# Kernel optimization log

Hardware: AMD Instinct MI355X
Metric: run time of the kernel (lower is better)

Reference implementation:

```python
import jax, jax.numpy as jnp
import numpy as np

NUM_CLASSES = 80
NUM_ANCHORS = 5
INPUT_SIZE = 6656
GRID = 208
CONF_THR = 0.5
IOU_THR = 0.5
TOPK = 1024  # pre-NMS cap (fixed-shape stand-in for the dynamic python NMS loop)
ANCHORS = np.array([[1.3221, 1.73145], [3.19275, 4.00944], [5.05587, 8.09892],
                    [9.47112, 4.84053], [11.2364, 10.0071]], dtype=np.float32)


def setup_inputs() -> dict:
    key = jax.random.key(0)
    x = jax.random.normal(key, (1, NUM_ANCHORS * (5 + NUM_CLASSES), GRID, GRID), dtype=jnp.float32)
    return {"x": x, "scaled_anchors": jnp.asarray(ANCHORS)}


def _decode(x, anchors):
    B, C, H, W = x.shape
    A = anchors.shape[0]
    stride_h = INPUT_SIZE / H
    stride_w = INPUT_SIZE / W
    # [B, A, H, W, 5+nc]
    p = x.reshape(B, A, C // A, H, W).transpose(0, 1, 3, 4, 2)
    bx = jax.nn.sigmoid(p[..., 0]) + jnp.arange(W, dtype=x.dtype)[None, None, None, :]
    by = jax.nn.sigmoid(p[..., 1]) + jnp.arange(H, dtype=x.dtype)[None, None, :, None]
    bw = jnp.exp(p[..., 2]) * anchors[:, 0][None, :, None, None]
    bh = jnp.exp(p[..., 3]) * anchors[:, 1][None, :, None, None]
    conf = jax.nn.sigmoid(p[..., 4])
    # original applies sigmoid then argmax; sigmoid is monotone so argmax of logits is identical
    cls_idx = jnp.argmax(p[..., 5:], axis=-1)
    scale = jnp.array([stride_w, stride_h, stride_w, stride_h], dtype=x.dtype)
    boxes = jnp.stack([bx, by, bw, bh], axis=-1) * scale  # [B,A,H,W,4]
    return boxes.reshape(B, -1, 4), conf.reshape(B, -1), cls_idx.reshape(B, -1)


def _iou_cxcywh(b1, b2):
    # faithful to the original intersection_over_union, including its
    # (c - s)/2 parenthesization and abs() on areas
    x1min = (b1[..., 0] - b1[..., 2]) / 2.0
    y1min = (b1[..., 1] - b1[..., 3]) / 2.0
    x1max = (b1[..., 0] + b1[..., 2]) / 2.0
    y1max = (b1[..., 1] + b1[..., 3]) / 2.0
    x2min = (b2[..., 0] - b2[..., 2]) / 2.0
    y2min = (b2[..., 1] - b2[..., 3]) / 2.0
    x2max = (b2[..., 0] + b2[..., 2]) / 2.0
    y2max = (b2[..., 1] + b2[..., 3]) / 2.0
    inter = (jnp.clip(jnp.minimum(x1max, x2max) - jnp.maximum(x1min, x2min), 0)
             * jnp.clip(jnp.minimum(y1max, y2max) - jnp.maximum(y1min, y2min), 0))
    a1 = jnp.abs((x1max - x1min) * (y1max - y1min))
    a2 = jnp.abs((x2max - x2min) * (y2max - y2min))
    return inter / (a1 + a2 - inter + 1e-6)


def _nms(boxes, conf, cls_idx):
    # conf filter + sort-by-confidence expressed as a fixed-size top_k
    scores = jnp.where(conf > CONF_THR, conf, -1.0)
    top_scores, idx = jax.lax.top_k(scores, TOPK)
    b = boxes[idx]            # [K,4]
    c = conf[idx]             # [K]
    cl = cls_idx[idx]         # [K]
    keep0 = top_scores > CONF_THR
    order = jnp.arange(TOPK)

    def body(i, keep):
        ious = _iou_cxcywh(b[i], b)                     # [K]
        suppress = (ious >= IOU_THR) & (cl == cl[i]) & (order > i)
        return jnp.where(keep[i], keep & ~suppress, keep)

    keep = jax.lax.fori_loop(0, TOPK, body, keep0)
    out = jnp.concatenate([b, c[:, None], cl[:, None].astype(b.dtype)], axis=-1)  # [K,6]
    return jnp.where(keep[:, None], out, 0.0)


def reference(x, scaled_anchors):
    boxes, conf, cls_idx = _decode(x, scaled_anchors)
    return _nms(boxes[0], conf[0], cls_idx[0])
```

## Files before the change

### kernel.cpp

```cpp
#include <hip/hip_runtime.h>
#include <stdint.h>

#define N_LOC 216320
#define PLANE 43264
#define GRIDW 208
#define NCAP 2048
#define TOPK 1024

typedef unsigned long long u64;
typedef uint32_t u32;

#define OFF_KEYS      0u
#define OFF_HIST      865280u
#define OFF_CTR       881664u
#define OFF_CAND      881696u
#define OFF_SELIDX    898080u
#define OFF_CONF      902176u
#define OFF_BOX       906272u
#define OFF_CLS       922656u
#define OFF_NZ        926752u
#define OFF_SUP       926880u

__global__ void k_init(u32* hist, u32* ctr, u64* nz, float* conf) {
    int t = blockIdx.x * 256 + threadIdx.x;
    if (t < 4096) hist[t] = 0;
    if (t < 8) ctr[t] = 0;
    if (t < 16) nz[t] = 0;
    if (t < 1024) conf[t] = 0.0f;
}

__global__ void k_scores(const float* __restrict__ x, u32* keys, u32* hist) {
    int i = blockIdx.x * 256 + threadIdx.x;
    if (i >= N_LOC) return;
    int a = i / PLANE;
    int hw = i - a * PLANE;
    float v = x[(a * 85 + 4) * PLANE + hw];
    float cf = 1.0f / (1.0f + expf(-v));
    u32 key = (cf > 0.5f) ? __float_as_uint(cf) : 0u;
    keys[i] = key;
    if (key) {
        u32 bin = (key >= 0x3F800000u) ? 4095u : ((key >> 11) & 0xFFFu);
        atomicAdd(&hist[bin], 1u);
    }
}

__global__ void k_findbin(const u32* hist, u32* ctr) {
    __shared__ u32 lhist[4096];
    __shared__ u32 csum[256];
    int t = threadIdx.x;
    u32 s = 0;
    for (int b = 0; b < 16; b++) {
        u32 h = hist[t * 16 + b];
        lhist[t * 16 + b] = h;
        s += h;
    }
    csum[t] = s;
    __syncthreads();
    if (t == 0) {
        u32 acc = 0;
        int selB = 0;
        int c = 255;
        for (; c >= 0; c--) {
            if (acc + csum[c] >= (u32)TOPK) break;
            acc += csum[c];
        }
        if (c >= 0) {
            int b = c * 16 + 15;
            for (; b >= c * 16; b--) {
                acc += lhist[b];
                if (acc >= (u32)TOPK) break;
            }
            if (b < c * 16) b = c * 16;
            selB = b;
        }
        ctr[1] = 0x3F000000u | ((u32)selB << 11);
    }
}

__global__ void k_compact(const u32* keys, u32* ctr, u64* cand) {
    int i = blockIdx.x * 256 + threadIdx.x;
    if (i >= N_LOC) return;
    u32 k = keys[i];
    u32 thr = ctr[1];
    if (k >= thr && k != 0u) {
        u32 pos = atomicAdd(&ctr[0], 1u);
        if (pos < (u32)NCAP)
            cand[pos] = ((u64)k << 32) | (u64)(~(u32)i);
    }
}

__global__ void __launch_bounds__(256) k_rank(const u32* __restrict__ ctr,
                                              const u64* __restrict__ cand,
                                              u32* sel_idx, float* conf) {
    u32 M = ctr[0];
    if (M > (u32)NCAP) M = NCAP;
    u32 b = blockIdx.x;
    if (b >= M) return;
    u64 key = cand[b];
    int t = threadIdx.x;
    u32 cnt = 0;
    for (u32 j = (u32)t; j < M; j += 256) cnt += (cand[j] > key) ? 1u : 0u;
    for (int off = 32; off; off >>= 1) cnt += __shfl_down(cnt, off);
    __shared__ u32 scnt;
    if (t == 0) scnt = 0;
    __syncthreads();
    if ((t & 63) == 0) atomicAdd(&scnt, cnt);
    __syncthreads();
    if (t == 0) {
        u32 rank = scnt;
        if (rank < (u32)TOPK) {
            sel_idx[rank] = ~((u32)key);
            conf[rank] = __uint_as_float((u32)(key >> 32));
        }
    }
}

__global__ void __launch_bounds__(256) k_decode(const float* __restrict__ x,
                                                const float* __restrict__ anchors,
                                                const u32* __restrict__ sel_idx,
                                                const float* __restrict__ conf,
                                                float4* box, float* clsf) {
    int wave = (blockIdx.x * 256 + threadIdx.x) >> 6;
    int lane = threadIdx.x & 63;
    float cf = conf[wave];
    if (cf <= 0.0f) {
        if (lane == 0) { box[wave] = make_float4(0.f, 0.f, 0.f, 0.f); clsf[wave] = 0.f; }
        return;
    }
    u32 i = sel_idx[wave];
    u32 a = i / PLANE;
    u32 hw = i - a * PLANE;
    u32 h = hw / GRIDW;
    u32 w = hw - h * GRIDW;
    const float* base = x + (size_t)(a * 85u) * PLANE + hw;
    float v0 = base[(5 + lane) * PLANE];
    int   c0 = lane;
    if (lane < 16) {
        float v1 = base[(5 + 64 + lane) * PLANE];
        if (v1 > v0) { v0 = v1; c0 = 64 + lane; }
    }
    float pv = (lane < 4) ? base[lane * PLANE] : 0.f;
    for (int off = 32; off; off >>= 1) {
        float ov = __shfl_xor(v0, off);
        int   oc = __shfl_xor(c0, off);
        if (ov > v0 || (ov == v0 && oc < c0)) { v0 = ov; c0 = oc; }
    }
    float p0 = __shfl(pv, 0);
    float p1 = __shfl(pv, 1);
    float p2 = __shfl(pv, 2);
    float p3 = __shfl(pv, 3);
    if (lane == 0) {
        float bx = (1.0f / (1.0f + expf(-p0)) + (float)w) * 32.0f;
        float by = (1.0f / (1.0f + expf(-p1)) + (float)h) * 32.0f;
        float bw = (expf(p2) * anchors[a * 2 + 0]) * 32.0f;
        float bh = (expf(p3) * anchors[a * 2 + 1]) * 32.0f;
        box[wave] = make_float4(bx, by, bw, bh);
        clsf[wave] = (float)c0;
    }
}

__global__ void __launch_bounds__(256) k_supmat(const float4* __restrict__ box,
                                                const float* __restrict__ clsf,
                                                u64* sup, u64* nz) {
    int i = blockIdx.x;
    float4 bi = box[i];
    float ci = clsf[i];
    float x1min = (bi.x - bi.z) * 0.5f, x1max = (bi.x + bi.z) * 0.5f;
    float y1min = (bi.y - bi.w) * 0.5f, y1max = (bi.y + bi.w) * 0.5f;
    float a1 = fabsf((x1max - x1min) * (y1max - y1min));
    int t = threadIdx.x;
    u64 any = 0;
    __shared__ u64 wany[4];
    for (int c = 0; c < 4; c++) {
        int j = c * 256 + t;
        bool s = false;
        if (j > i) {
            float4 bj = box[j];
            float x2min = (bj.x - bj.z) * 0.5f, x2max = (bj.x + bj.z) * 0.5f;
            float y2min = (bj.y - bj.w) * 0.5f, y2max = (bj.y + bj.w) * 0.5f;
            float iw = fmaxf(fminf(x1max, x2max) - fmaxf(x1min, x2min), 0.0f);
            float ih = fmaxf(fminf(y1max, y2max) - fmaxf(y1min, y2min), 0.0f);
            float inter = iw * ih;
            float a2 = fabsf((x2max - x2min) * (y2max - y2min));
            float iou = inter / (a1 + a2 - inter + 1e-6f);
            s = (iou >= 0.5f) && (clsf[j] == ci);
        }
        u64 msk = __ballot(s);
        if ((t & 63) == 0) sup[i * 16 + c * 4 + (t >> 6)] = msk;
        any |= msk;
    }
    if ((t & 63) == 0) wany[t >> 6] = any;
    __syncthreads();
    if (t == 0) {
        u64 tot = wany[0] | wany[1] | wany[2] | wany[3];
        if (tot) atomicOr(&nz[i >> 6], 1ull << (i & 63));
    }
}

__global__ void __launch_bounds__(1024) k_nms_out(const u64* __restrict__ sup,
                                                  const u64* __restrict__ nz,
                                                  const float4* __restrict__ box,
                                                  const float* __restrict__ conf,
                                                  const float* __restrict__ clsf,
                                                  float* __restrict__ out) {
    __shared__ u64 candLDS[16];
    __shared__ u64 remLDS[16];
    int t = threadIdx.x;
    float cf = conf[t];
    bool valid = cf > 0.0f;
    u64 bm = __ballot(valid);
    if ((t & 63) == 0) candLDS[t >> 6] = bm;
    __syncthreads();
    if (t < 64) {
        int lane = t;
        u64 rem = 0;
        u64 cnd = (lane < 16) ? candLDS[lane] : 0ull;
        u64 nzw = (lane < 16) ? nz[lane] : 0ull;
        for (int g = 0; g < 16; g++) {
            u64 myword = cnd & ~rem;
            u64 live = __shfl(myword, g);
            u64 act = live & __shfl(nzw, g);
            while (act) {
                int b = __builtin_ctzll(act);
                int i = g * 64 + b;
                u64 row = (lane < 16) ? sup[i * 16 + lane] : 0ull;
                rem |= row;
                u64 row_g = __shfl(row, g);
                act &= ~row_g;
                act &= ~(1ull << b);
            }
        }
        if (lane < 16) remLDS[lane] = rem;
    }
    __syncthreads();
    int r = t;
    u64 rw = remLDS[r >> 6];
    bool kept = valid && !((rw >> (r & 63)) & 1ull);
    float4 b4 = box[r];
    float cl = clsf[r];
    float* o = out + r * 6;
    if (kept) {
        o[0] = b4.x; o[1] = b4.y; o[2] = b4.z; o[3] = b4.w; o[4] = cf; o[5] = cl;
    } else {
        o[0] = 0.f; o[1] = 0.f; o[2] = 0.f; o[3] = 0.f; o[4] = 0.f; o[5] = 0.f;
    }
}

extern "C" void kernel_launch(void* const* d_in, const int* in_sizes, int n_in,
                              void* d_out, int out_size, void* d_ws, size_t ws_size,
                              hipStream_t stream) {
    const float* x = (const float*)d_in[0];
    const float* anchors = (const float*)d_in[1];
    float* out = (float*)d_out;
    char* ws = (char*)d_ws;

    u32* keys     = (u32*)(ws + OFF_KEYS);
    u32* hist     = (u32*)(ws + OFF_HIST);
    u32* ctr      = (u32*)(ws + OFF_CTR);
    u64* cand     = (u64*)(ws + OFF_CAND);
    u32* sel_idx  = (u32*)(ws + OFF_SELIDX);
    float* conf   = (float*)(ws + OFF_CONF);
    float4* box   = (float4*)(ws + OFF_BOX);
    float* clsf   = (float*)(ws + OFF_CLS);
    u64* nz       = (u64*)(ws + OFF_NZ);
    u64* sup      = (u64*)(ws + OFF_SUP);

    k_init<<<16, 256, 0, stream>>>(hist, ctr, nz, conf);
    k_scores<<<(N_LOC + 255) / 256, 256, 0, stream>>>(x, keys, hist);
    k_findbin<<<1, 256, 0, stream>>>(hist, ctr);
    k_compact<<<(N_LOC + 255) / 256, 256, 0, stream>>>(keys, ctr, cand);
    k_rank<<<NCAP, 256, 0, stream>>>(ctr, cand, sel_idx, conf);
    k_decode<<<256, 256, 0, stream>>>(x, anchors, sel_idx, conf, box, clsf);
    k_supmat<<<TOPK, 256, 0, stream>>>(box, clsf, sup, nz);
    k_nms_out<<<1, 1024, 0, stream>>>(sup, nz, box, conf, clsf, out);
}
```

Before: 138.0 us.

## Fuse pipeline stages via last-block patterns and merge rank with decode

Cuts the launch chain from eight kernels to a memset plus four. The bin search now runs in the last block of the score kernel, and the NMS scan runs in the last block of the suppression-matrix kernel, both using atomic completion counters. Rank and decode are merged into one 64-thread-per-candidate kernel. The suppression kernel stages boxes and classes in shared memory and handles four rows per block. This removes launch and serialization overhead, at the cost of more memory-ordering complexity and a tail phase that runs in a single block.

```diff
diff --git a/kernel.cpp b/kernel.cpp
--- a/kernel.cpp
+++ b/kernel.cpp
@@ -10,28 +10,27 @@
 typedef unsigned long long u64;
 typedef uint32_t u32;
 
-#define OFF_KEYS      0u
-#define OFF_HIST      865280u
-#define OFF_CTR       881664u
-#define OFF_CAND      881696u
-#define OFF_SELIDX    898080u
-#define OFF_CONF      902176u
-#define OFF_BOX       906272u
-#define OFF_CLS       922656u
-#define OFF_NZ        926752u
-#define OFF_SUP       926880u
-
-__global__ void k_init(u32* hist, u32* ctr, u64* nz, float* conf) {
-    int t = blockIdx.x * 256 + threadIdx.x;
-    if (t < 4096) hist[t] = 0;
-    if (t < 8) ctr[t] = 0;
-    if (t < 16) nz[t] = 0;
-    if (t < 1024) conf[t] = 0.0f;
-}
-
-__global__ void k_scores(const float* __restrict__ x, u32* keys, u32* hist) {
+#define OFF_BOX       0u
+#define OFF_HIST      16384u
+#define OFF_CONF      32768u
+#define OFF_CLS       36864u
+#define OFF_NZ        40960u
+#define OFF_CTR       41088u
+#define META_BYTES    41152u
+#define OFF_CAND      41152u
+#define OFF_SUP       57536u
+#define OFF_KEYS      188608u
+
+__device__ __forceinline__ u32 aload32(const u32* p) {
+    return __hip_atomic_load(p, __ATOMIC_RELAXED, __HIP_MEMORY_SCOPE_AGENT);
+}
+__device__ __forceinline__ u64 aload64(const u64* p) {
+    return __hip_atomic_load(p, __ATOMIC_RELAXED, __HIP_MEMORY_SCOPE_AGENT);
+}
+
+__global__ void __launch_bounds__(256) k_scores(const float* __restrict__ x,
+                                                u32* keys, u32* hist, u32* ctr) {
     int i = blockIdx.x * 256 + threadIdx.x;
-    if (i >= N_LOC) return;
     int a = i / PLANE;
     int hw = i - a * PLANE;
     float v = x[(a * 85 + 4) * PLANE + hw];
@@ -42,15 +41,22 @@
         u32 bin = (key >= 0x3F800000u) ? 4095u : ((key >> 11) & 0xFFFu);
         atomicAdd(&hist[bin], 1u);
     }
-}
-
-__global__ void k_findbin(const u32* hist, u32* ctr) {
+    __shared__ int isLast;
+    __syncthreads();
+    if (threadIdx.x == 0) {
+        __threadfence();
+        u32 old = atomicAdd(&ctr[2], 1u);
+        isLast = (old == gridDim.x - 1u);
+    }
+    __syncthreads();
+    if (!isLast) return;
+    __threadfence();
     __shared__ u32 lhist[4096];
     __shared__ u32 csum[256];
     int t = threadIdx.x;
     u32 s = 0;
     for (int b = 0; b < 16; b++) {
-        u32 h = hist[t * 16 + b];
+        u32 h = aload32(&hist[t * 16 + b]);
         lhist[t * 16 + b] = h;
         s += h;
     }
@@ -77,57 +83,35 @@
     }
 }
 
-__global__ void k_compact(const u32* keys, u32* ctr, u64* cand) {
+__global__ void __launch_bounds__(256) k_compact(const u32* __restrict__ keys,
+                                                 u32* ctr, u64* cand) {
     int i = blockIdx.x * 256 + threadIdx.x;
-    if (i >= N_LOC) return;
     u32 k = keys[i];
     u32 thr = ctr[1];
-    if (k >= thr && k != 0u) {
+    if (k >= thr) {
         u32 pos = atomicAdd(&ctr[0], 1u);
         if (pos < (u32)NCAP)
             cand[pos] = ((u64)k << 32) | (u64)(~(u32)i);
     }
 }
 
-__global__ void __launch_bounds__(256) k_rank(const u32* __restrict__ ctr,
-                                              const u64* __restrict__ cand,
-                                              u32* sel_idx, float* conf) {
+__global__ void __launch_bounds__(64) k_rankdec(const float* __restrict__ x,
+                                                const float* __restrict__ anchors,
+                                                const u32* __restrict__ ctr,
+                                                const u64* __restrict__ cand,
+                                                float4* box, float* conf, float* clsf) {
     u32 M = ctr[0];
     if (M > (u32)NCAP) M = NCAP;
     u32 b = blockIdx.x;
     if (b >= M) return;
     u64 key = cand[b];
-    int t = threadIdx.x;
+    int lane = threadIdx.x;
     u32 cnt = 0;
-    for (u32 j = (u32)t; j < M; j += 256) cnt += (cand[j] > key) ? 1u : 0u;
-    for (int off = 32; off; off >>= 1) cnt += __shfl_down(cnt, off);
-    __shared__ u32 scnt;
-    if (t == 0) scnt = 0;
-    __syncthreads();
-    if ((t & 63) == 0) atomicAdd(&scnt, cnt);
-    __syncthreads();
-    if (t == 0) {
-        u32 rank = scnt;
-        if (rank < (u32)TOPK) {
-            sel_idx[rank] = ~((u32)key);
-            conf[rank] = __uint_as_float((u32)(key >> 32));
-        }
-    }
-}
-
-__global__ void __launch_bounds__(256) k_decode(const float* __restrict__ x,
-                                                const float* __restrict__ anchors,
-                                                const u32* __restrict__ sel_idx,
-                                                const float* __restrict__ conf,
-                                                float4* box, float* clsf) {
-    int wave = (blockIdx.x * 256 + threadIdx.x) >> 6;
-    int lane = threadIdx.x & 63;
-    float cf = conf[wave];
-    if (cf <= 0.0f) {
-        if (lane == 0) { box[wave] = make_float4(0.f, 0.f, 0.f, 0.f); clsf[wave] = 0.f; }
-        return;
-    }
-    u32 i = sel_idx[wave];
+    for (u32 j = (u32)lane; j < M; j += 64) cnt += (cand[j] > key) ? 1u : 0u;
+    for (int off = 32; off; off >>= 1) cnt += __shfl_xor(cnt, off);
+    if (cnt >= (u32)TOPK) return;
+    u32 rank = cnt;
+    u32 i = ~((u32)key);
     u32 a = i / PLANE;
     u32 hw = i - a * PLANE;
     u32 h = hw / GRIDW;
@@ -154,95 +138,118 @@
         float by = (1.0f / (1.0f + expf(-p1)) + (float)h) * 32.0f;
         float bw = (expf(p2) * anchors[a * 2 + 0]) * 32.0f;
         float bh = (expf(p3) * anchors[a * 2 + 1]) * 32.0f;
-        box[wave] = make_float4(bx, by, bw, bh);
-        clsf[wave] = (float)c0;
-    }
-}
-
-__global__ void __launch_bounds__(256) k_supmat(const float4* __restrict__ box,
-                                                const float* __restrict__ clsf,
-                                                u64* sup, u64* nz) {
-    int i = blockIdx.x;
-    float4 bi = box[i];
-    float ci = clsf[i];
-    float x1min = (bi.x - bi.z) * 0.5f, x1max = (bi.x + bi.z) * 0.5f;
-    float y1min = (bi.y - bi.w) * 0.5f, y1max = (bi.y + bi.w) * 0.5f;
-    float a1 = fabsf((x1max - x1min) * (y1max - y1min));
+        box[rank] = make_float4(bx, by, bw, bh);
+        conf[rank] = __uint_as_float((u32)(key >> 32));
+        clsf[rank] = (float)c0;
+    }
+}
+
+__global__ void __launch_bounds__(256) k_sup_nms(const float4* __restrict__ box,
+                                                 const float* __restrict__ clsf,
+                                                 const float* __restrict__ conf,
+                                                 u64* sup, u64* nz, u32* ctr,
+                                                 float* __restrict__ out) {
+    __shared__ float4 sbox[1024];
+    __shared__ float  scls[1024];
+    __shared__ u64 wany[4];
     int t = threadIdx.x;
-    u64 any = 0;
-    __shared__ u64 wany[4];
     for (int c = 0; c < 4; c++) {
         int j = c * 256 + t;
-        bool s = false;
-        if (j > i) {
-            float4 bj = box[j];
-            float x2min = (bj.x - bj.z) * 0.5f, x2max = (bj.x + bj.z) * 0.5f;
-            float y2min = (bj.y - bj.w) * 0.5f, y2max = (bj.y + bj.w) * 0.5f;
-            float iw = fmaxf(fminf(x1max, x2max) - fmaxf(x1min, x2min), 0.0f);
-            float ih = fmaxf(fminf(y1max, y2max) - fmaxf(y1min, y2min), 0.0f);
-            float inter = iw * ih;
-            float a2 = fabsf((x2max - x2min) * (y2max - y2min));
-            float iou = inter / (a1 + a2 - inter + 1e-6f);
-            s = (iou >= 0.5f) && (clsf[j] == ci);
-        }
-        u64 msk = __ballot(s);
-        if ((t & 63) == 0) sup[i * 16 + c * 4 + (t >> 6)] = msk;
-        any |= msk;
-    }
-    if ((t & 63) == 0) wany[t >> 6] = any;
-    __syncthreads();
+        sbox[j] = box[j];
+        scls[j] = clsf[j];
+    }
+    __syncthreads();
+    u32 rowflags = 0;
+    for (int r = 0; r < 4; r++) {
+        int i = blockIdx.x * 4 + r;
+        float4 bi = sbox[i];
+        float ci = scls[i];
+        float x1min = (bi.x - bi.z) * 0.5f, x1max = (bi.x + bi.z) * 0.5f;
+        float y1min = (bi.y - bi.w) * 0.5f, y1max = (bi.y + bi.w) * 0.5f;
+        float a1 = fabsf((x1max - x1min) * (y1max - y1min));
+        u64 any = 0;
+        for (int c = 0; c < 4; c++) {
+            int j = c * 256 + t;
+            bool sfl = false;
+            if (j > i) {
+                float4 bj = sbox[j];
+                float x2min = (bj.x - bj.z) * 0.5f, x2max = (bj.x + bj.z) * 0.5f;
+                float y2min = (bj.y - bj.w) * 0.5f, y2max = (bj.y + bj.w) * 0.5f;
+                float iw = fmaxf(fminf(x1max, x2max) - fmaxf(x1min, x2min), 0.0f);
+                float ih = fmaxf(fminf(y1max, y2max) - fmaxf(y1min, y2min), 0.0f);
+                float inter = iw * ih;
+                float a2 = fabsf((x2max - x2min) * (y2max - y2min));
+                float iou = inter / (a1 + a2 - inter + 1e-6f);
+                sfl = (iou >= 0.5f) && (scls[j] == ci);
+            }
+            u64 msk = __ballot(sfl);
+            if ((t & 63) == 0) sup[i * 16 + c * 4 + (t >> 6)] = msk;
+            any |= msk;
+        }
+        if ((t & 63) == 0) wany[t >> 6] = any;
+        __syncthreads();
+        if (t == 0) {
+            if (wany[0] | wany[1] | wany[2] | wany[3]) rowflags |= 1u << r;
+        }
+        __syncthreads();
+    }
+    __shared__ int isLast;
     if (t == 0) {
-        u64 tot = wany[0] | wany[1] | wany[2] | wany[3];
-        if (tot) atomicOr(&nz[i >> 6], 1ull << (i & 63));
-    }
-}
-
-__global__ void __launch_bounds__(1024) k_nms_out(const u64* __restrict__ sup,
-                                                  const u64* __restrict__ nz,
-                                                  const float4* __restrict__ box,
-                                                  const float* __restrict__ conf,
-                                                  const float* __restrict__ clsf,
-                                                  float* __restrict__ out) {
+        if (rowflags)
+            atomicOr(&nz[(4u * blockIdx.x) >> 6], (u64)rowflags << ((4u * blockIdx.x) & 63u));
+        __threadfence();
+        u32 old = atomicAdd(&ctr[3], 1u);
+        isLast = (old == gridDim.x - 1u);
+    }
+    __syncthreads();
+    if (!isLast) return;
+    __threadfence();
     __shared__ u64 candLDS[16];
+    __shared__ u64 nzLDS[16];
     __shared__ u64 remLDS[16];
-    int t = threadIdx.x;
-    float cf = conf[t];
-    bool valid = cf > 0.0f;
-    u64 bm = __ballot(valid);
-    if ((t & 63) == 0) candLDS[t >> 6] = bm;
+    for (int c = 0; c < 4; c++) {
+        bool valid = conf[c * 256 + t] > 0.0f;
+        u64 bm = __ballot(valid);
+        if ((t & 63) == 0) candLDS[c * 4 + (t >> 6)] = bm;
+    }
+    if (t < 16) nzLDS[t] = aload64(&nz[t]);
     __syncthreads();
     if (t < 64) {
         int lane = t;
         u64 rem = 0;
         u64 cnd = (lane < 16) ? candLDS[lane] : 0ull;
-        u64 nzw = (lane < 16) ? nz[lane] : 0ull;
+        u64 nzw = (lane < 16) ? nzLDS[lane] : 0ull;
         for (int g = 0; g < 16; g++) {
             u64 myword = cnd & ~rem;
             u64 live = __shfl(myword, g);
             u64 act = live & __shfl(nzw, g);
             while (act) {
-                int b = __builtin_ctzll(act);
-                int i = g * 64 + b;
-                u64 row = (lane < 16) ? sup[i * 16 + lane] : 0ull;
+                int bb = __builtin_ctzll(act);
+                int i2 = g * 64 + bb;
+                u64 row = (lane < 16) ? aload64(&sup[i2 * 16 + lane]) : 0ull;
                 rem |= row;
                 u64 row_g = __shfl(row, g);
                 act &= ~row_g;
-                act &= ~(1ull << b);
+                act &= ~(1ull << bb);
             }
         }
         if (lane < 16) remLDS[lane] = rem;
     }
     __syncthreads();
-    int r = t;
-    u64 rw = remLDS[r >> 6];
-    bool kept = valid && !((rw >> (r & 63)) & 1ull);
-    float4 b4 = box[r];
-    float cl = clsf[r];
-    float* o = out + r * 6;
-    if (kept) {
-        o[0] = b4.x; o[1] = b4.y; o[2] = b4.z; o[3] = b4.w; o[4] = cf; o[5] = cl;
-    } else {
-        o[0] = 0.f; o[1] = 0.f; o[2] = 0.f; o[3] = 0.f; o[4] = 0.f; o[5] = 0.f;
+    for (int c = 0; c < 4; c++) {
+        int r = c * 256 + t;
+        u64 cw = candLDS[r >> 6];
+        u64 rw = remLDS[r >> 6];
+        bool kept = ((cw >> (r & 63)) & 1ull) && !((rw >> (r & 63)) & 1ull);
+        float4 b4 = sbox[r];
+        float cf = conf[r];
+        float cl = scls[r];
+        float* o = out + r * 6;
+        if (kept) {
+            o[0] = b4.x; o[1] = b4.y; o[2] = b4.z; o[3] = b4.w; o[4] = cf; o[5] = cl;
+        } else {
+            o[0] = 0.f; o[1] = 0.f; o[2] = 0.f; o[3] = 0.f; o[4] = 0.f; o[5] = 0.f;
+        }
     }
 }
 
@@ -254,23 +261,19 @@
     float* out = (float*)d_out;
     char* ws = (char*)d_ws;
 
-    u32* keys     = (u32*)(ws + OFF_KEYS);
+    float4* box   = (float4*)(ws + OFF_BOX);
     u32* hist     = (u32*)(ws + OFF_HIST);
+    float* conf   = (float*)(ws + OFF_CONF);
+    float* clsf   = (float*)(ws + OFF_CLS);
+    u64* nz       = (u64*)(ws + OFF_NZ);
     u32* ctr      = (u32*)(ws + OFF_CTR);
     u64* cand     = (u64*)(ws + OFF_CAND);
-    u32* sel_idx  = (u32*)(ws + OFF_SELIDX);
-    float* conf   = (float*)(ws + OFF_CONF);
-    float4* box   = (float4*)(ws + OFF_BOX);
-    float* clsf   = (float*)(ws + OFF_CLS);
-    u64* nz       = (u64*)(ws + OFF_NZ);
     u64* sup      = (u64*)(ws + OFF_SUP);
-
-    k_init<<<16, 256, 0, stream>>>(hist, ctr, nz, conf);
-    k_scores<<<(N_LOC + 255) / 256, 256, 0, stream>>>(x, keys, hist);
-    k_findbin<<<1, 256, 0, stream>>>(hist, ctr);
-    k_compact<<<(N_LOC + 255) / 256, 256, 0, stream>>>(keys, ctr, cand);
-    k_rank<<<NCAP, 256, 0, stream>>>(ctr, cand, sel_idx, conf);
-    k_decode<<<256, 256, 0, stream>>>(x, anchors, sel_idx, conf, box, clsf);
-    k_supmat<<<TOPK, 256, 0, stream>>>(box, clsf, sup, nz);
-    k_nms_out<<<1, 1024, 0, stream>>>(sup, nz, box, conf, clsf, out);
-}
+    u32* keys     = (u32*)(ws + OFF_KEYS);
+
+    hipMemsetAsync(ws, 0, META_BYTES, stream);
+    k_scores<<<N_LOC / 256, 256, 0, stream>>>(x, keys, hist, ctr);
+    k_compact<<<N_LOC / 256, 256, 0, stream>>>(keys, ctr, cand);
+    k_rankdec<<<NCAP, 64, 0, stream>>>(x, anchors, ctr, cand, box, conf, clsf);
+    k_sup_nms<<<256, 256, 0, stream>>>(box, clsf, conf, sup, nz, ctr, out);
+}
```

Result: slower. 157.7 us (+14.3%).
